# Optimization experiments

Measured on AMD Instinct MI355X. Metric: run time of the kernel, lower is better.

Reference implementation:

```python
import jax, jax.numpy as jnp
import numpy as np
from jax import lax

# Fixed image shape (H, W) for all images, standard detection resize
H_IMG, W_IMG = 800.0, 1333.0
SCORE_THRESH = 0.05
NMS_THRESH = 0.5
DET_PER_IMG = 100
K_PRE = 2048  # NMS candidate budget per image (after score threshold)
BBOX_XFORM_CLIP = float(np.log(1000.0 / 16.0))
WX, WY, WW, WH = 10.0, 10.0, 5.0, 5.0  # bbox_reg_weights


def setup_inputs() -> dict:
    B, P, C = 8, 2000, 81
    key = jax.random.key(0)
    k1, k2, k3, k4 = jax.random.split(key, 4)
    class_logits = 2.0 * jax.random.normal(k1, (B * P, C), jnp.float32)
    box_regression = 0.5 * jax.random.normal(k2, (B * P, C * 4), jnp.float32)
    # valid proposal boxes inside the image: (x1,y1) + (w,h)
    xy = jax.random.uniform(k3, (B, P, 2), jnp.float32) * jnp.array([W_IMG - 128.0, H_IMG - 128.0], jnp.float32)
    wh = 1.0 + 127.0 * jax.random.uniform(k4, (B, P, 2), jnp.float32)
    proposals = jnp.concatenate([xy, xy + wh], axis=-1)
    return {"class_logits": class_logits, "box_regression": box_regression, "proposals": proposals}


def _decode(rel, boxes):
    # BoxCoder.decode: rel [N, C, 4], boxes [N, 4] -> [N, C, 4]
    w = boxes[:, 2] - boxes[:, 0]
    h = boxes[:, 3] - boxes[:, 1]
    cx = boxes[:, 0] + 0.5 * w
    cy = boxes[:, 1] + 0.5 * h
    dx = rel[..., 0] / WX
    dy = rel[..., 1] / WY
    dw = jnp.minimum(rel[..., 2] / WW, BBOX_XFORM_CLIP)
    dh = jnp.minimum(rel[..., 3] / WH, BBOX_XFORM_CLIP)
    pcx = dx * w[:, None] + cx[:, None]
    pcy = dy * h[:, None] + cy[:, None]
    pw = jnp.exp(dw) * w[:, None]
    ph = jnp.exp(dh) * h[:, None]
    return jnp.stack([pcx - 0.5 * pw, pcy - 0.5 * ph, pcx + 0.5 * pw, pcy + 0.5 * ph], axis=-1)


def _pairwise_iou(b):
    # b: [K, 4] -> [K, K]
    area = jnp.maximum(b[:, 2] - b[:, 0], 0.0) * jnp.maximum(b[:, 3] - b[:, 1], 0.0)
    lt = jnp.maximum(b[:, None, :2], b[None, :, :2])
    rb = jnp.minimum(b[:, None, 2:], b[None, :, 2:])
    wh = jnp.maximum(rb - lt, 0.0)
    inter = wh[..., 0] * wh[..., 1]
    union = area[:, None] + area[None, :] - inter
    return inter / jnp.maximum(union, 1e-9)


def _greedy_nms(boxes, valid):
    # boxes: [K, 4] sorted by score desc; valid: [K] bool. Exact greedy NMS.
    K = boxes.shape[0]
    iou = _pairwise_iou(boxes)
    idx = jnp.arange(K)

    def body(i, keep):
        sup = keep[i] & (iou[i] > NMS_THRESH) & (idx > i)
        return keep & ~sup

    return lax.fori_loop(0, K, body, valid)


def reference(class_logits, box_regression, proposals):
    B, P, _ = proposals.shape
    C = class_logits.shape[-1]
    # decode all class-specific boxes, softmax scores
    rel = box_regression.reshape(-1, C, 4)
    pred = _decode(rel, proposals.reshape(-1, 4)).reshape(B, P, C, 4)
    scores = jax.nn.softmax(class_logits, axis=-1).reshape(B, P, C)
    # drop background class 0
    M = P * (C - 1)
    boxes = pred[:, :, 1:, :].reshape(B, M, 4)
    scores = scores[:, :, 1:].reshape(B, M)
    labels = jnp.broadcast_to(jnp.arange(1, C)[None, None, :], (B, P, C - 1)).reshape(B, M)
    # clip to image
    x1 = jnp.clip(boxes[..., 0], 0.0, W_IMG)
    y1 = jnp.clip(boxes[..., 1], 0.0, H_IMG)
    x2 = jnp.clip(boxes[..., 2], 0.0, W_IMG)
    y2 = jnp.clip(boxes[..., 3], 0.0, H_IMG)
    boxes = jnp.stack([x1, y1, x2, y2], axis=-1)
    # score threshold + remove_small_boxes(min_size=0.01), as a validity mask
    valid = (scores > SCORE_THRESH) & ((x2 - x1) >= 0.01) & ((y2 - y1) >= 0.01)
    masked = jnp.where(valid, scores, -1.0)
    # top-K candidates per image (sorted desc -> NMS visiting order)
    top_s, top_i = lax.top_k(masked, K_PRE)
    top_b = jnp.take_along_axis(boxes, top_i[..., None], axis=1)
    top_l = jnp.take_along_axis(labels, top_i, axis=1)
    top_v = top_s > 0.0
    # batched_nms: per-class coordinate offsets so classes never overlap
    off = top_l.astype(jnp.float32) * (jnp.maximum(W_IMG, H_IMG) + 1.0)
    keep = jax.vmap(_greedy_nms)(top_b + off[..., None], top_v)
    final = jnp.where(keep, top_s, -1.0)
    det_s, det_i = lax.top_k(final, DET_PER_IMG)
    det_b = jnp.take_along_axis(top_b, det_i[..., None], axis=1)
    det_l = jnp.take_along_axis(top_l, det_i, axis=1)
    det_valid = det_s > 0.0  # padding slots have score -1
    return det_b, det_s, det_l, det_valid
```

## Files before the change

### kernel.cpp

```cpp
#include <hip/hip_runtime.h>
#include <cstdint>
#include <cstddef>

typedef unsigned long long u64;

constexpr int Bn   = 8;
constexpr int Pn   = 2000;
constexpr int Cn   = 81;
constexpr int CM1  = 80;
constexpr int KPRE = 2048;
constexpr int NDET = 100;
constexpr int SECP = 8;
constexpr int NSEC2 = Pn / SECP;
constexpr int SSLOT = 160;
constexpr int CAP  = 4096;
constexpr int NBINS = 5632;
constexpr int BINOFF = (122 << 10);
constexpr float W_IMG = 1333.0f;
constexpr float H_IMG = 800.0f;
constexpr float XFORM_CLIP = 4.135166556742356f;
constexpr float NMS_OFF = 1334.0f;

constexpr size_t OFF_HIST = 0;
constexpr size_t ZERO_BYTES = (size_t)Bn * NBINS * 4;
constexpr size_t OFF_SL   = ZERO_BYTES;
constexpr size_t OFF_SC   = OFF_SL + (size_t)Bn * NSEC2 * SSLOT * 8;
constexpr size_t OFF_CANDA = OFF_SC + (size_t)Bn * NSEC2 * 4;

__device__ __forceinline__ void decode_clip(const float4 rv, float w, float h,
                                            float cx, float cy, float out[4]) {
  float dx = rv.x / 10.0f;
  float dy = rv.y / 10.0f;
  float dw = fminf(rv.z / 5.0f, XFORM_CLIP);
  float dh = fminf(rv.w / 5.0f, XFORM_CLIP);
  float pcx = dx * w + cx;
  float pcy = dy * h + cy;
  float pw = expf(dw) * w;
  float ph = expf(dh) * h;
  out[0] = fminf(fmaxf(pcx - 0.5f * pw, 0.0f), W_IMG);
  out[1] = fminf(fmaxf(pcy - 0.5f * ph, 0.0f), H_IMG);
  out[2] = fminf(fmaxf(pcx + 0.5f * pw, 0.0f), W_IMG);
  out[3] = fminf(fmaxf(pcy + 0.5f * ph, 0.0f), H_IMG);
}

__device__ __forceinline__ int score_bin(unsigned bits) {
  int bin = (int)(bits >> 13) - BINOFF;
  return min(max(bin, 0), NBINS - 1);
}

__device__ __forceinline__ void key_decode(u64 key, int b,
                                           const float* __restrict__ reg,
                                           const float* __restrict__ props,
                                           float bx[4], int& label, float& sc) {
  sc = __uint_as_float((unsigned)(key >> 32));
  bx[0] = bx[1] = bx[2] = bx[3] = 0.0f;
  label = 0;
  if (key != 0ull) {
    int m = (int)(0xFFFFFFFFu - (unsigned)key);
    int p = m / CM1;
    int c = m - p * CM1 + 1;
    int nidx = b * Pn + p;
    const float4 pb = *reinterpret_cast<const float4*>(props + (size_t)nidx * 4);
    float w = pb.z - pb.x, h = pb.w - pb.y;
    float cx = pb.x + 0.5f * w, cy = pb.y + 0.5f * h;
    float4 rv = *reinterpret_cast<const float4*>(reg + (size_t)nidx * (Cn * 4) + c * 4);
    decode_clip(rv, w, h, cx, cy, bx);
    label = c;
  }
}

__global__ __launch_bounds__(256) void
k1_score(const float* __restrict__ logits, const float* __restrict__ reg,
         const float* __restrict__ props, u64* __restrict__ slices,
         int* __restrict__ scnt, int* __restrict__ hist) {
  int blk = blockIdx.x, t = threadIdx.x, lane = t & 63, wv = t >> 6;
  int b = blk / NSEC2, sec = blk % NSEC2;
  __shared__ u64 cbuf[SSLOT];
  __shared__ int cnt_sh;
  if (t == 0) cnt_sh = 0;
  __syncthreads();
  int* hrow = hist + (size_t)b * NBINS;

  #pragma unroll
  for (int pp = wv; pp < SECP; pp += 4) {
    int p = sec * SECP + pp;
    int wid = b * Pn + p;
    const float* lg = logits + (size_t)wid * Cn;
    float x0 = lg[lane];
    float x1 = (lane < Cn - 64) ? lg[64 + lane] : -3.4e38f;
    float mx = fmaxf(x0, x1);
    for (int m = 32; m; m >>= 1) mx = fmaxf(mx, __shfl_xor(mx, m, 64));
    float e0 = expf(x0 - mx);
    float e1 = (lane < Cn - 64) ? expf(x1 - mx) : 0.0f;
    float ssum = e0 + e1;
    for (int m = 32; m; m >>= 1) ssum += __shfl_xor(ssum, m, 64);

    const float4 pb = *reinterpret_cast<const float4*>(props + (size_t)wid * 4);
    float w = pb.z - pb.x, h = pb.w - pb.y;
    float cx = pb.x + 0.5f * w, cy = pb.y + 0.5f * h;
    const float* rrow = reg + (size_t)wid * (Cn * 4);

    u64 key0 = 0ull, key1 = 0ull;
    if (lane >= 1) {
      float sc = e0 / ssum;
      if (sc > 0.05f) {
        float4 rv = *reinterpret_cast<const float4*>(rrow + lane * 4);
        float bx[4];
        decode_clip(rv, w, h, cx, cy, bx);
        if ((bx[2] - bx[0] >= 0.01f) && (bx[3] - bx[1] >= 0.01f)) {
          unsigned m = (unsigned)(p * CM1 + (lane - 1));
          key0 = ((u64)__float_as_uint(sc) << 32) | (0xFFFFFFFFu - m);
        }
      }
    }
    if (lane < Cn - 64) {
      int c = 64 + lane;
      float sc = e1 / ssum;
      if (sc > 0.05f) {
        float4 rv = *reinterpret_cast<const float4*>(rrow + c * 4);
        float bx[4];
        decode_clip(rv, w, h, cx, cy, bx);
        if ((bx[2] - bx[0] >= 0.01f) && (bx[3] - bx[1] >= 0.01f)) {
          unsigned m = (unsigned)(p * CM1 + (c - 1));
          key1 = ((u64)__float_as_uint(sc) << 32) | (0xFFFFFFFFu - m);
        }
      }
    }
    u64 bal0 = __ballot(key0 != 0ull);
    u64 bal1 = __ballot(key1 != 0ull);
    int tot = __popcll(bal0) + __popcll(bal1);
    if (tot) {
      int base = 0;
      if (lane == 0) base = atomicAdd(&cnt_sh, tot);
      base = __shfl(base, 0, 64);
      int r0 = __popcll(bal0 & ((1ull << lane) - 1ull));
      int r1 = __popcll(bal0) + __popcll(bal1 & ((1ull << lane) - 1ull));
      if (key0) {
        cbuf[base + r0] = key0;
        atomicAdd(&hrow[score_bin((unsigned)(key0 >> 32))], 1);
      }
      if (key1) {
        cbuf[base + r1] = key1;
        atomicAdd(&hrow[score_bin((unsigned)(key1 >> 32))], 1);
      }
    }
  }
  __syncthreads();
  int n = cnt_sh;
  for (int i = t; i < n; i += 256) slices[(size_t)blk * SSLOT + i] = cbuf[i];
  if (t == 0) scnt[blk] = n;
}

__global__ __launch_bounds__(1024) void
k2c_compact(const int* __restrict__ hist, const u64* __restrict__ slices,
            const int* __restrict__ scnt, u64* __restrict__ candA) {
  int b = blockIdx.x, t = threadIdx.x, lane = t & 63, wv = t >> 6;
  __shared__ int partial[256];
  __shared__ int sufAfter[256];
  __shared__ int lcnt[NSEC2];
  __shared__ int tmax_sh, cnt_sh;
  const int CH = NBINS / 256;
  const int* hrow = hist + (size_t)b * NBINS;

  if (t == 0) { tmax_sh = 0; cnt_sh = 0; }
  if (t < 256) {
    int lo = t * CH, hi = lo + CH;
    int s = 0;
    for (int i = lo; i < hi; i++) s += hrow[i];
    partial[t] = s;
  }
  if (t < NSEC2) lcnt[t] = scnt[b * NSEC2 + t];
  __syncthreads();
  if (t == 0) {
    int acc = 0;
    for (int q = 255; q >= 0; q--) { sufAfter[q] = acc; acc += partial[q]; }
  }
  __syncthreads();
  if (t < 256) {
    int lo = t * CH, hi = lo + CH;
    int cum = sufAfter[t];
    int cand = -1;
    for (int i = hi - 1; i >= lo; i--) {
      cum += hrow[i];
      if (cum >= KPRE) { cand = i; break; }
    }
    if (cand >= 0) atomicMax(&tmax_sh, cand);
  }
  __syncthreads();
  int T = tmax_sh;

  for (int sec = wv; sec < NSEC2; sec += 16) {
    int n = lcnt[sec];
    const u64* sl = slices + (size_t)(b * NSEC2 + sec) * SSLOT;
    for (int i0 = 0; i0 < n; i0 += 64) {
      int i = i0 + lane;
      u64 key = (i < n) ? sl[i] : 0ull;
      bool pass = key && (score_bin((unsigned)(key >> 32)) >= T);
      u64 bal = __ballot(pass);
      int tot = __popcll(bal);
      if (tot) {
        int base = 0;
        if (lane == 0) base = atomicAdd(&cnt_sh, tot);
        base = __shfl(base, 0, 64);
        int rank = __popcll(bal & ((1ull << lane) - 1ull));
        int pos = base + rank;
        if (pass && pos < CAP) candA[(size_t)b * CAP + pos] = key;
      }
    }
  }
  __syncthreads();
  for (int i = min(cnt_sh, CAP) + t; i < CAP; i += 1024)
    candA[(size_t)b * CAP + i] = 0ull;
}

__global__ __launch_bounds__(256) void
k4a_chunk(u64* __restrict__ candA) {
  __shared__ u64 sk[512];
  int blk = blockIdx.x, t = threadIdx.x;
  int b = blk >> 3, ch = blk & 7;
  int base = ch * 512;
  #pragma unroll
  for (int i = t; i < 512; i += 256) sk[i] = candA[(size_t)b * CAP + base + i];
  __syncthreads();
  for (int k = 2; k <= 512; k <<= 1) {
    for (int j = k >> 1; j > 0; j >>= 1) {
      #pragma unroll
      for (int i = t; i < 512; i += 256) {
        int ixj = i ^ j;
        if (ixj > i) {
          u64 a = sk[i], c2 = sk[ixj];
          bool dir = ((i & k) == 0);
          if ((a < c2) == dir) { sk[i] = c2; sk[ixj] = a; }
        }
      }
      __syncthreads();
    }
  }
  #pragma unroll
  for (int i = t; i < 512; i += 256)
    candA[(size_t)b * CAP + base + i] = sk[i];
}

template <int CHV>
__device__ __forceinline__ void mp_round(u64* buf, int base, int nA, int nB,
                                         int outLen, int tid) {
  const u64* A = buf + base;
  const u64* B = buf + base + nA;
  int d = tid * CHV;
  u64 rg[CHV];
  int cnt = 0;
  if (d < outLen) {
    int lo = max(0, d - nB), hi = min(d, nA);
    while (lo < hi) {
      int mid = (lo + hi) >> 1;
      if (A[mid] >= B[d - 1 - mid]) lo = mid + 1; else hi = mid;
    }
    int i = lo, j = d - lo;
    for (int e = 0; e < CHV && d + e < outLen; e++) {
      u64 v;
      if (j >= nB || (i < nA && A[i] >= B[j])) v = A[i++];
      else v = B[j++];
      rg[cnt++] = v;
    }
  }
  __syncthreads();
  for (int e = 0; e < cnt; e++) buf[base + d + e] = rg[e];
  __syncthreads();
}

__global__ __launch_bounds__(1024) void
k5_merge_nms(u64* __restrict__ candA, const float* __restrict__ reg,
             const float* __restrict__ props, float* __restrict__ out) {
  int b = blockIdx.x, t = threadIdx.x, lane = t & 63, w = t >> 6;
  __shared__ u64 bufA[CAP];
  __shared__ u64 maskb[256][4];
  __shared__ u64 keepw[KPRE / 64];
  __shared__ int accI[NDET];
  __shared__ int kcnt_sh;
  float4* obox = (float4*)bufA;

  #pragma unroll
  for (int s = 0; s < 4; s++) {
    int i = t + s * 1024;
    bufA[i] = candA[(size_t)b * CAP + i];
  }
  __syncthreads();
  mp_round<4>(bufA, (t >> 8) * 1024, 512, 512, 1024, t & 255);
  mp_round<4>(bufA, (t >> 9) * 2048, 1024, 1024, 2048, t & 511);
  mp_round<2>(bufA, 0, 2048, 2048, 2048, t);

  u64 k0 = bufA[t], k1 = bufA[t + 1024];
  candA[(size_t)b * CAP + t] = k0;
  candA[(size_t)b * CAP + t + 1024] = k1;
  {
    u64 bal = __ballot(k0 != 0ull);
    if (lane == 0) keepw[w] = bal;
    bal = __ballot(k1 != 0ull);
    if (lane == 0) keepw[16 + w] = bal;
  }
  __syncthreads();
  #pragma unroll
  for (int s = 0; s < 2; s++) {
    int j = t + s * 1024;
    u64 key = s ? k1 : k0;
    float bx[4]; int label; float sc;
    key_decode(key, b, reg, props, bx, label, sc);
    float off = (float)label * NMS_OFF;
    obox[j] = make_float4(bx[0] + off, bx[1] + off, bx[2] + off, bx[3] + off);
  }
  __syncthreads();

  int kcount = 0;
  for (int w0 = 0; w0 < KPRE && kcount < NDET; w0 += 256) {
    if (w0 > 0 && kcount > 0) {
      if (t < 256) {
        int j = w0 + t;
        u64 kwv = keepw[j >> 6];
        bool alive = (kwv >> (j & 63)) & 1ull;
        if (alive) {
          float4 jb = obox[j];
          float jar = fmaxf(jb.z - jb.x, 0.0f) * fmaxf(jb.w - jb.y, 0.0f);
          for (int a = 0; a < kcount; a++) {
            float4 ab = obox[accI[a]];
            float ix1 = fmaxf(ab.x, jb.x), iy1 = fmaxf(ab.y, jb.y);
            float ix2 = fminf(ab.z, jb.z), iy2 = fminf(ab.w, jb.w);
            float iw = fmaxf(ix2 - ix1, 0.0f), ih = fmaxf(iy2 - iy1, 0.0f);
            float inter = iw * ih;
            if (inter > 0.0f) {
              float aar = fmaxf(ab.z - ab.x, 0.0f) * fmaxf(ab.w - ab.y, 0.0f);
              float iou = inter / fmaxf(aar + jar - inter, 1e-9f);
              if (iou > 0.5f) { alive = false; break; }
            }
          }
        }
        u64 bal = __ballot(alive);
        if (lane == 0) keepw[(w0 >> 6) + (t >> 6)] = bal;
      }
      __syncthreads();
    }
    {
      int r = t >> 2, wd = t & 3;
      int rgp = w0 + r;
      bool ralive = (keepw[rgp >> 6] >> (rgp & 63)) & 1ull;
      float4 rb = obox[rgp];
      float rar = fmaxf(rb.z - rb.x, 0.0f) * fmaxf(rb.w - rb.y, 0.0f);
      u64 m = 0;
      if (ralive) {
        int cb0 = w0 + wd * 64;
        for (int jj = 0; jj < 64; jj++) {
          int cg = cb0 + jj;
          float4 cb = obox[cg];
          float ix1 = fmaxf(rb.x, cb.x), iy1 = fmaxf(rb.y, cb.y);
          float ix2 = fminf(rb.z, cb.z), iy2 = fminf(rb.w, cb.w);
          float iw = fmaxf(ix2 - ix1, 0.0f), ih = fmaxf(iy2 - iy1, 0.0f);
          float inter = iw * ih;
          if (inter > 0.0f && cg > rgp) {
            float car = fmaxf(cb.z - cb.x, 0.0f) * fmaxf(cb.w - cb.y, 0.0f);
            float iou = inter / fmaxf(rar + car - inter, 1e-9f);
            if (iou > 0.5f) m |= (1ull << jj);
          }
        }
      }
      maskb[r][wd] = m;
    }
    __syncthreads();
    if (w == 0) {
      u64 kw0 = keepw[(w0 >> 6) + 0];
      u64 kw1 = keepw[(w0 >> 6) + 1];
      u64 kw2 = keepw[(w0 >> 6) + 2];
      u64 kw3 = keepw[(w0 >> 6) + 3];
      int kc = kcount;
      #pragma unroll
      for (int wq = 0; wq < 4; wq++) {
        u64 cw = (wq == 0) ? kw0 : (wq == 1) ? kw1 : (wq == 2) ? kw2 : kw3;
        if (cw == 0ull) continue;
        for (int rb0 = 0; rb0 < 64 && kc < NDET; rb0 += 4) {
          u64 gbits = (cw >> rb0) & 0xFull;
          int r = wq * 64 + rb0;
          u64 rm0a = maskb[r][0],   rm0b = maskb[r][1],   rm0c = maskb[r][2],   rm0d = maskb[r][3];
          u64 rm1a = maskb[r+1][0], rm1b = maskb[r+1][1], rm1c = maskb[r+1][2], rm1d = maskb[r+1][3];
          u64 rm2a = maskb[r+2][0], rm2b = maskb[r+2][1], rm2c = maskb[r+2][2], rm2d = maskb[r+2][3];
          u64 rm3a = maskb[r+3][0], rm3b = maskb[r+3][1], rm3c = maskb[r+3][2], rm3d = maskb[r+3][3];
          if (gbits == 0ull) continue;
          #pragma unroll
          for (int d = 0; d < 4; d++) {
            u64 cwq = (wq == 0) ? kw0 : (wq == 1) ? kw1 : (wq == 2) ? kw2 : kw3;
            if ((cwq >> (rb0 + d)) & 1ull) {
              if (lane == 0) accI[kc] = w0 + r + d;
              kc++;
              if (kc >= NDET) break;
              u64 ma = (d == 0) ? rm0a : (d == 1) ? rm1a : (d == 2) ? rm2a : rm3a;
              u64 mb = (d == 0) ? rm0b : (d == 1) ? rm1b : (d == 2) ? rm2b : rm3b;
              u64 mc = (d == 0) ? rm0c : (d == 1) ? rm1c : (d == 2) ? rm2c : rm3c;
              u64 md = (d == 0) ? rm0d : (d == 1) ? rm1d : (d == 2) ? rm2d : rm3d;
              kw0 &= ~ma; kw1 &= ~mb; kw2 &= ~mc; kw3 &= ~md;
            }
          }
          cw = (wq == 0) ? kw0 : (wq == 1) ? kw1 : (wq == 2) ? kw2 : kw3;
        }
      }
      if (lane == 0) {
        keepw[(w0 >> 6) + 0] = kw0;
        keepw[(w0 >> 6) + 1] = kw1;
        keepw[(w0 >> 6) + 2] = kw2;
        keepw[(w0 >> 6) + 3] = kw3;
        kcnt_sh = kc;
      }
    }
    __syncthreads();
    kcount = kcnt_sh;
  }

  if (t == 0 && kcount < NDET) {
    int run = kcount;
    for (int wq = 0; wq < KPRE / 64 && run < NDET; wq++) {
      u64 nk = ~keepw[wq];
      while (nk && run < NDET) {
        int bit2 = __ffsll((long long)nk) - 1;
        nk &= nk - 1;
        accI[run++] = wq * 64 + bit2;
      }
    }
  }
  __syncthreads();

  if (t < NDET) {
    int k = accI[t];
    bool kept = t < kcount;
    u64 key = candA[(size_t)b * CAP + k];
    float bx[4]; int label; float sc;
    key_decode(key, b, reg, props, bx, label, sc);
    int oi = b * NDET + t;
    out[(size_t)oi * 4 + 0] = bx[0];
    out[(size_t)oi * 4 + 1] = bx[1];
    out[(size_t)oi * 4 + 2] = bx[2];
    out[(size_t)oi * 4 + 3] = bx[3];
    out[Bn * NDET * 4 + oi] = kept ? sc : -1.0f;
    out[Bn * NDET * 5 + oi] = (float)label;
    out[Bn * NDET * 6 + oi] = kept ? 1.0f : 0.0f;
  }
}

extern "C" void kernel_launch(void* const* d_in, const int* in_sizes, int n_in,
                              void* d_out, int out_size, void* d_ws, size_t ws_size,
                              hipStream_t stream) {
  const float* logits = (const float*)d_in[0];
  const float* reg    = (const float*)d_in[1];
  const float* props  = (const float*)d_in[2];
  float* out = (float*)d_out;
  char* ws = (char*)d_ws;

  int* hist   = (int*)(ws + OFF_HIST);
  u64* slices = (u64*)(ws + OFF_SL);
  int* scnt   = (int*)(ws + OFF_SC);
  u64* candA  = (u64*)(ws + OFF_CANDA);

  hipMemsetAsync(ws + OFF_HIST, 0, ZERO_BYTES, stream);
  k1_score<<<Bn * NSEC2, 256, 0, stream>>>(logits, reg, props, slices, scnt, hist);
  k2c_compact<<<Bn, 1024, 0, stream>>>(hist, slices, scnt, candA);
  k4a_chunk<<<Bn * 8, 256, 0, stream>>>(candA);
  k5_merge_nms<<<Bn, 1024, 0, stream>>>(candA, reg, props, out);
}
```

Baseline: 139.7 us.

## Fuse histogram, threshold compaction and chunk sort into one LDS-resident kernel

Removes the global score histogram, so the first kernel no longer does global atomics and the memset goes away. The histogram is now rebuilt in shared memory inside a new select kernel, which also does the compaction and the 512-element bitonic chunk sorts in LDS before writing candA once. This cuts a memset and a kernel launch, plus a global round trip of candA. In exchange, the histogram, select and sort work runs on only 8 blocks instead of spreading the sort over 64 blocks, and the select kernel needs roughly 56KB of LDS.

```diff
diff --git a/kernel.cpp b/kernel.cpp
--- a/kernel.cpp
+++ b/kernel.cpp
@@ -21,9 +21,7 @@
 constexpr float XFORM_CLIP = 4.135166556742356f;
 constexpr float NMS_OFF = 1334.0f;
 
-constexpr size_t OFF_HIST = 0;
-constexpr size_t ZERO_BYTES = (size_t)Bn * NBINS * 4;
-constexpr size_t OFF_SL   = ZERO_BYTES;
+constexpr size_t OFF_SL   = 0;
 constexpr size_t OFF_SC   = OFF_SL + (size_t)Bn * NSEC2 * SSLOT * 8;
 constexpr size_t OFF_CANDA = OFF_SC + (size_t)Bn * NSEC2 * 4;
 
@@ -72,14 +70,13 @@
 __global__ __launch_bounds__(256) void
 k1_score(const float* __restrict__ logits, const float* __restrict__ reg,
          const float* __restrict__ props, u64* __restrict__ slices,
-         int* __restrict__ scnt, int* __restrict__ hist) {
+         int* __restrict__ scnt) {
   int blk = blockIdx.x, t = threadIdx.x, lane = t & 63, wv = t >> 6;
   int b = blk / NSEC2, sec = blk % NSEC2;
   __shared__ u64 cbuf[SSLOT];
   __shared__ int cnt_sh;
   if (t == 0) cnt_sh = 0;
   __syncthreads();
-  int* hrow = hist + (size_t)b * NBINS;
 
   #pragma unroll
   for (int pp = wv; pp < SECP; pp += 4) {
@@ -135,14 +132,8 @@
       base = __shfl(base, 0, 64);
       int r0 = __popcll(bal0 & ((1ull << lane) - 1ull));
       int r1 = __popcll(bal0) + __popcll(bal1 & ((1ull << lane) - 1ull));
-      if (key0) {
-        cbuf[base + r0] = key0;
-        atomicAdd(&hrow[score_bin((unsigned)(key0 >> 32))], 1);
-      }
-      if (key1) {
-        cbuf[base + r1] = key1;
-        atomicAdd(&hrow[score_bin((unsigned)(key1 >> 32))], 1);
-      }
+      if (key0) cbuf[base + r0] = key0;
+      if (key1) cbuf[base + r1] = key1;
     }
   }
   __syncthreads();
@@ -152,40 +143,57 @@
 }
 
 __global__ __launch_bounds__(1024) void
-k2c_compact(const int* __restrict__ hist, const u64* __restrict__ slices,
-            const int* __restrict__ scnt, u64* __restrict__ candA) {
+k2s_select(const u64* __restrict__ slices, const int* __restrict__ scnt,
+           u64* __restrict__ candA) {
   int b = blockIdx.x, t = threadIdx.x, lane = t & 63, wv = t >> 6;
+  __shared__ int histL[NBINS];
+  __shared__ u64 candL[CAP];
+  __shared__ int lcnt[NSEC2];
   __shared__ int partial[256];
   __shared__ int sufAfter[256];
-  __shared__ int lcnt[NSEC2];
   __shared__ int tmax_sh, cnt_sh;
+
+  for (int i = t; i < NBINS; i += 1024) histL[i] = 0;
+  if (t < NSEC2) lcnt[t] = scnt[b * NSEC2 + t];
+  if (t == 0) { tmax_sh = 0; cnt_sh = 0; }
+  __syncthreads();
+
+  for (int sec = wv; sec < NSEC2; sec += 16) {
+    int n = lcnt[sec];
+    const u64* sl = slices + (size_t)(b * NSEC2 + sec) * SSLOT;
+    for (int i = lane; i < n; i += 64)
+      atomicAdd(&histL[score_bin((unsigned)(sl[i] >> 32))], 1);
+  }
+  __syncthreads();
+
   const int CH = NBINS / 256;
-  const int* hrow = hist + (size_t)b * NBINS;
-
-  if (t == 0) { tmax_sh = 0; cnt_sh = 0; }
   if (t < 256) {
     int lo = t * CH, hi = lo + CH;
     int s = 0;
-    for (int i = lo; i < hi; i++) s += hrow[i];
+    for (int i = lo; i < hi; i++) s += histL[i];
     partial[t] = s;
   }
-  if (t < NSEC2) lcnt[t] = scnt[b * NSEC2 + t];
-  __syncthreads();
-  if (t == 0) {
-    int acc = 0;
-    for (int q = 255; q >= 0; q--) { sufAfter[q] = acc; acc += partial[q]; }
-  }
-  __syncthreads();
+  __syncthreads();
+  if (t < 256) sufAfter[t] = partial[t];
+  __syncthreads();
+  for (int s = 1; s < 256; s <<= 1) {
+    int y = 0;
+    if (t < 256 && t + s < 256) y = sufAfter[t + s];
+    __syncthreads();
+    if (t < 256) sufAfter[t] += y;
+    __syncthreads();
+  }
   if (t < 256) {
     int lo = t * CH, hi = lo + CH;
-    int cum = sufAfter[t];
+    int cum = (t + 1 < 256) ? sufAfter[t + 1] : 0;
     int cand = -1;
     for (int i = hi - 1; i >= lo; i--) {
-      cum += hrow[i];
+      cum += histL[i];
       if (cum >= KPRE) { cand = i; break; }
     }
     if (cand >= 0) atomicMax(&tmax_sh, cand);
   }
+  for (int i = t; i < CAP; i += 1024) candL[i] = 0ull;
   __syncthreads();
   int T = tmax_sh;
 
@@ -204,41 +212,33 @@
         base = __shfl(base, 0, 64);
         int rank = __popcll(bal & ((1ull << lane) - 1ull));
         int pos = base + rank;
-        if (pass && pos < CAP) candA[(size_t)b * CAP + pos] = key;
-      }
-    }
-  }
-  __syncthreads();
-  for (int i = min(cnt_sh, CAP) + t; i < CAP; i += 1024)
-    candA[(size_t)b * CAP + i] = 0ull;
-}
-
-__global__ __launch_bounds__(256) void
-k4a_chunk(u64* __restrict__ candA) {
-  __shared__ u64 sk[512];
-  int blk = blockIdx.x, t = threadIdx.x;
-  int b = blk >> 3, ch = blk & 7;
-  int base = ch * 512;
-  #pragma unroll
-  for (int i = t; i < 512; i += 256) sk[i] = candA[(size_t)b * CAP + base + i];
-  __syncthreads();
+        if (pass && pos < CAP) candL[pos] = key;
+      }
+    }
+  }
+  __syncthreads();
+
   for (int k = 2; k <= 512; k <<= 1) {
     for (int j = k >> 1; j > 0; j >>= 1) {
       #pragma unroll
-      for (int i = t; i < 512; i += 256) {
+      for (int s = 0; s < 4; s++) {
+        int i = t + s * 1024;
         int ixj = i ^ j;
         if (ixj > i) {
-          u64 a = sk[i], c2 = sk[ixj];
-          bool dir = ((i & k) == 0);
-          if ((a < c2) == dir) { sk[i] = c2; sk[ixj] = a; }
+          u64 a = candL[i], c2 = candL[ixj];
+          bool dir = (((i & 511) & k) == 0);
+          if ((a < c2) == dir) { candL[i] = c2; candL[ixj] = a; }
         }
       }
       __syncthreads();
     }
   }
+
   #pragma unroll
-  for (int i = t; i < 512; i += 256)
-    candA[(size_t)b * CAP + base + i] = sk[i];
+  for (int s = 0; s < 4; s++) {
+    int i = t + s * 1024;
+    candA[(size_t)b * CAP + i] = candL[i];
+  }
 }
 
 template <int CHV>
@@ -450,14 +450,11 @@
   float* out = (float*)d_out;
   char* ws = (char*)d_ws;
 
-  int* hist   = (int*)(ws + OFF_HIST);
   u64* slices = (u64*)(ws + OFF_SL);
   int* scnt   = (int*)(ws + OFF_SC);
   u64* candA  = (u64*)(ws + OFF_CANDA);
 
-  hipMemsetAsync(ws + OFF_HIST, 0, ZERO_BYTES, stream);
-  k1_score<<<Bn * NSEC2, 256, 0, stream>>>(logits, reg, props, slices, scnt, hist);
-  k2c_compact<<<Bn, 1024, 0, stream>>>(hist, slices, scnt, candA);
-  k4a_chunk<<<Bn * 8, 256, 0, stream>>>(candA);
+  k1_score<<<Bn * NSEC2, 256, 0, stream>>>(logits, reg, props, slices, scnt);
+  k2s_select<<<Bn, 1024, 0, stream>>>(slices, scnt, candA);
   k5_merge_nms<<<Bn, 1024, 0, stream>>>(candA, reg, props, out);
 }
```

Result: slower. 152.5 us (+9.1%).
